# Optimization experiments

Measured on AMD Instinct MI355X. Metric: run time of the kernel, lower is better.

Reference implementation:

```python
import jax, jax.numpy as jnp
import numpy as np

T, B, INPUT_SIZE, NUM_NEURONS, OUTPUT_SIZE = 200, 256, 784, 1024, 10
TAU_M, V_REST, THRESH0, TAU_THRESH, BETA, DT = 20.0, -65.0, -50.0, 100.0, 5.0, 1.0


def setup_inputs() -> dict:
    key = jax.random.key(0)
    k1, k2, k3 = jax.random.split(key, 3)
    input_spikes = jax.random.uniform(k1, (T, B, INPUT_SIZE), dtype=jnp.float32)
    input_weights = jax.random.uniform(k2, (INPUT_SIZE, NUM_NEURONS), dtype=jnp.float32)
    # W_rec = -0.5 * (ones - eye): lateral inhibition buffer
    W_rec = -0.5 * (jnp.ones((NUM_NEURONS, NUM_NEURONS), jnp.float32) - jnp.eye(NUM_NEURONS, dtype=jnp.float32))
    output_weights = jax.random.uniform(k3, (NUM_NEURONS, OUTPUT_SIZE), dtype=jnp.float32)
    return {"input_spikes": input_spikes, "input_weights": input_weights,
            "W_rec": W_rec, "output_weights": output_weights}


def reference(input_spikes, input_weights, W_rec, output_weights):
    Bd = input_spikes.shape[1]
    n = input_weights.shape[1]
    mp0 = jnp.full((Bd, n), V_REST, jnp.float32)       # membrane potential
    th0 = jnp.full((Bd, n), THRESH0, jnp.float32)      # dynamic threshold
    h0 = jnp.zeros((Bd, n), jnp.float32)               # previous hidden spikes

    def step(carry, x_t):
        mp, th, prev = carry
        net = x_t @ input_weights + prev @ W_rec        # (B, n)
        mp = mp + (V_REST - mp) / TAU_M + net * DT
        spikes = (mp >= th).astype(jnp.float32)
        th = th + BETA * spikes - (th - THRESH0) / TAU_THRESH * DT
        mp = jnp.where(spikes > 0, V_REST, mp)          # reset on spike
        return (mp, th, spikes), spikes

    _, hidden_spikes = jax.lax.scan(step, (mp0, th0, h0), input_spikes)  # (T, B, n)
    spike_counts = hidden_spikes.sum(axis=0)            # (B, n)
    logits = spike_counts @ output_weights              # (B, out)
    return logits, hidden_spikes
```

## Files before the change

### kernel.cpp

```cpp
#include <hip/hip_runtime.h>


#define TT 200
#define BB 256
#define KK 784
#define NN 1024
#define OO 10

__device__ __forceinline__ float shfl_down64(float v, int d) {
  return __shfl_down(v, d, 64);
}

__global__ __launch_bounds__(256)
void gemm_net(const float* __restrict__ X, const float* __restrict__ W,
              float* __restrict__ C) {
  __shared__ float As[16][64];
  __shared__ float Bs[16][64];
  const int tid = threadIdx.x;
  const int m0 = blockIdx.x * 64;
  const int n0 = blockIdx.y * 64;
  const int tr = (tid >> 4) * 4;
  const int tc = (tid & 15) * 4;
  const int arow = tid >> 2;
  const int ak   = (tid & 3) * 4;
  const int brow = tid >> 4;
  const int bc   = (tid & 15) * 4;

  float acc[4][4] = {};

  for (int k0 = 0; k0 < KK; k0 += 16) {
    float4 av = *(const float4*)(X + (m0 + arow) * KK + k0 + ak);
    float4 bv = *(const float4*)(W + (k0 + brow) * NN + n0 + bc);
    __syncthreads();
    As[ak + 0][arow] = av.x;
    As[ak + 1][arow] = av.y;
    As[ak + 2][arow] = av.z;
    As[ak + 3][arow] = av.w;
    *(float4*)&Bs[brow][bc] = bv;
    __syncthreads();
#pragma unroll
    for (int k = 0; k < 16; ++k) {
      float4 a = *(const float4*)&As[k][tr];
      float4 b = *(const float4*)&Bs[k][tc];
      float aa[4] = {a.x, a.y, a.z, a.w};
      float bb[4] = {b.x, b.y, b.z, b.w};
#pragma unroll
      for (int i = 0; i < 4; ++i)
#pragma unroll
        for (int j = 0; j < 4; ++j)
          acc[i][j] = fmaf(aa[i], bb[j], acc[i][j]);
    }
  }
#pragma unroll
  for (int i = 0; i < 4; ++i) {
    float4 v = {acc[i][0], acc[i][1], acc[i][2], acc[i][3]};
    *(float4*)(C + (m0 + tr + i) * NN + n0 + tc) = v;
  }
}

__global__ __launch_bounds__(256)
void snn_scan(float* __restrict__ hid, const float* __restrict__ Wout,
              float* __restrict__ logits) {
  constexpr float V_REST = -65.0f, THRESH0 = -50.0f, TAU_M = 20.0f,
                  TAU_TH = 100.0f, BETA = 5.0f, DT = 1.0f;
  const int b = blockIdx.x;
  const int tid = threadIdx.x;
  __shared__ float s_part[4];
  __shared__ float s_log[4][OO];

  float mp[4], th[4], prev[4], cnt[4], net[4];
#pragma unroll
  for (int k = 0; k < 4; ++k) {
    mp[k] = V_REST; th[k] = THRESH0; prev[k] = 0.0f; cnt[k] = 0.0f;
  }
  float S = 0.0f;
  const int base = b * NN + tid;

#pragma unroll
  for (int k = 0; k < 4; ++k) net[k] = hid[base + k * 256];

  for (int t = 0; t < TT; ++t) {
    float local = 0.0f;
    float sp[4];
#pragma unroll
    for (int k = 0; k < 4; ++k) {
      float rec = -0.5f * (S - prev[k]);
      float nv  = net[k] + rec;
      float m   = mp[k] + (V_REST - mp[k]) / TAU_M;
      m = m + nv * DT;
      float s = (m >= th[k]) ? 1.0f : 0.0f;
      th[k] = (th[k] + BETA * s) - ((th[k] - THRESH0) / TAU_TH) * DT;
      mp[k] = (s > 0.0f) ? V_REST : m;
      cnt[k] += s;
      prev[k] = s;
      sp[k] = s;
      local += s;
    }
    const int off = t * (BB * NN) + base;
#pragma unroll
    for (int k = 0; k < 4; ++k) hid[off + k * 256] = sp[k];

    if (t + 1 < TT) {
      const int noff = (t + 1) * (BB * NN) + base;
#pragma unroll
      for (int k = 0; k < 4; ++k) net[k] = hid[noff + k * 256];
    }

#pragma unroll
    for (int d = 32; d > 0; d >>= 1) local += shfl_down64(local, d);
    __syncthreads();
    if ((tid & 63) == 0) s_part[tid >> 6] = local;
    __syncthreads();
    S = s_part[0] + s_part[1] + s_part[2] + s_part[3];
  }

  float lg[OO];
#pragma unroll
  for (int o = 0; o < OO; ++o) lg[o] = 0.0f;
#pragma unroll
  for (int k = 0; k < 4; ++k) {
    const int j = tid + k * 256;
#pragma unroll
    for (int o = 0; o < OO; ++o) lg[o] = fmaf(cnt[k], Wout[j * OO + o], lg[o]);
  }
#pragma unroll
  for (int o = 0; o < OO; ++o) {
    float v = lg[o];
#pragma unroll
    for (int d = 32; d > 0; d >>= 1) v += shfl_down64(v, d);
    if ((tid & 63) == 0) s_log[tid >> 6][o] = v;
  }
  __syncthreads();
  if (tid < OO)
    logits[b * OO + tid] =
        s_log[0][tid] + s_log[1][tid] + s_log[2][tid] + s_log[3][tid];
}

extern "C" void kernel_launch(void* const* d_in, const int* in_sizes, int n_in,
                              void* d_out, int out_size, void* d_ws,
                              size_t ws_size, hipStream_t stream) {
  const float* X    = (const float*)d_in[0];
  const float* Win  = (const float*)d_in[1];
  const float* Wout = (const float*)d_in[3];

  float* logits = (float*)d_out;
  float* hid    = (float*)d_out + BB * OO;

  dim3 g1(TT * BB / 64, NN / 64);
  gemm_net<<<g1, 256, 0, stream>>>(X, Win, hid);
  snn_scan<<<BB, 256, 0, stream>>>(hid, Wout, logits);
}
```

Baseline: 1.465 ms.

## Enlarge GEMM tiles to 128x128 and widen scan to one neuron per thread

The input-projection GEMM now computes 128x128 output tiles per block, with each thread holding an 8x8 register accumulator. This raises arithmetic intensity and cuts shared/global traffic per FMA, and the grid is reordered so N is the fast dimension. The scan kernel uses 1024 threads per batch row, one neuron each. It prefetches the net input two steps ahead, counts spikes with a wave ballot/popcount, and double-buffers the partial sums so each step needs only one barrier. The costs are higher register pressure in the GEMM and more waves per barrier in the scan.

```diff
diff --git a/kernel.cpp b/kernel.cpp
--- a/kernel.cpp
+++ b/kernel.cpp
@@ -7,133 +7,143 @@
 #define NN 1024
 #define OO 10
 
-__device__ __forceinline__ float shfl_down64(float v, int d) {
-  return __shfl_down(v, d, 64);
-}
-
 __global__ __launch_bounds__(256)
 void gemm_net(const float* __restrict__ X, const float* __restrict__ W,
               float* __restrict__ C) {
-  __shared__ float As[16][64];
-  __shared__ float Bs[16][64];
+  __shared__ float As[16][128];
+  __shared__ float Bs[16][128];
+  float4 (*As4)[32] = (float4(*)[32])As;
+  float4 (*Bs4)[32] = (float4(*)[32])Bs;
+
   const int tid = threadIdx.x;
-  const int m0 = blockIdx.x * 64;
-  const int n0 = blockIdx.y * 64;
-  const int tr = (tid >> 4) * 4;
-  const int tc = (tid & 15) * 4;
-  const int arow = tid >> 2;
-  const int ak   = (tid & 3) * 4;
-  const int brow = tid >> 4;
-  const int bc   = (tid & 15) * 4;
+  const int n0 = blockIdx.x * 128;
+  const int m0 = blockIdx.y * 128;
+  const int tx = tid & 15;
+  const int ty = tid >> 4;
+  const int arow = tid >> 1;
+  const int ak   = (tid & 1) * 8;
+  const int brow = tid >> 5;
+  const int bc   = (tid & 31) * 4;
 
-  float acc[4][4] = {};
+  float acc[2][2][4][4] = {};
 
   for (int k0 = 0; k0 < KK; k0 += 16) {
-    float4 av = *(const float4*)(X + (m0 + arow) * KK + k0 + ak);
-    float4 bv = *(const float4*)(W + (k0 + brow) * NN + n0 + bc);
+    const float* ap = X + (size_t)(m0 + arow) * KK + k0 + ak;
+    float4 a0 = *(const float4*)(ap);
+    float4 a1 = *(const float4*)(ap + 4);
+    float4 b0 = *(const float4*)(W + (size_t)(k0 + brow) * NN + n0 + bc);
+    float4 b1 = *(const float4*)(W + (size_t)(k0 + brow + 8) * NN + n0 + bc);
     __syncthreads();
-    As[ak + 0][arow] = av.x;
-    As[ak + 1][arow] = av.y;
-    As[ak + 2][arow] = av.z;
-    As[ak + 3][arow] = av.w;
-    *(float4*)&Bs[brow][bc] = bv;
+    As[ak + 0][arow] = a0.x;
+    As[ak + 1][arow] = a0.y;
+    As[ak + 2][arow] = a0.z;
+    As[ak + 3][arow] = a0.w;
+    As[ak + 4][arow] = a1.x;
+    As[ak + 5][arow] = a1.y;
+    As[ak + 6][arow] = a1.z;
+    As[ak + 7][arow] = a1.w;
+    *(float4*)&Bs[brow][bc] = b0;
+    *(float4*)&Bs[brow + 8][bc] = b1;
     __syncthreads();
 #pragma unroll
     for (int k = 0; k < 16; ++k) {
-      float4 a = *(const float4*)&As[k][tr];
-      float4 b = *(const float4*)&Bs[k][tc];
-      float aa[4] = {a.x, a.y, a.z, a.w};
-      float bb[4] = {b.x, b.y, b.z, b.w};
+      float4 A0 = As4[k][ty];
+      float4 A1 = As4[k][16 + ty];
+      float4 B0 = Bs4[k][tx];
+      float4 B1 = Bs4[k][16 + tx];
+      float a[2][4] = {{A0.x, A0.y, A0.z, A0.w}, {A1.x, A1.y, A1.z, A1.w}};
+      float b[2][4] = {{B0.x, B0.y, B0.z, B0.w}, {B1.x, B1.y, B1.z, B1.w}};
 #pragma unroll
-      for (int i = 0; i < 4; ++i)
+      for (int qi = 0; qi < 2; ++qi)
 #pragma unroll
-        for (int j = 0; j < 4; ++j)
-          acc[i][j] = fmaf(aa[i], bb[j], acc[i][j]);
+        for (int qj = 0; qj < 2; ++qj)
+#pragma unroll
+          for (int i = 0; i < 4; ++i)
+#pragma unroll
+            for (int j = 0; j < 4; ++j)
+              acc[qi][qj][i][j] = fmaf(a[qi][i], b[qj][j], acc[qi][qj][i][j]);
     }
   }
 #pragma unroll
-  for (int i = 0; i < 4; ++i) {
-    float4 v = {acc[i][0], acc[i][1], acc[i][2], acc[i][3]};
-    *(float4*)(C + (m0 + tr + i) * NN + n0 + tc) = v;
-  }
+  for (int qi = 0; qi < 2; ++qi)
+#pragma unroll
+    for (int i = 0; i < 4; ++i) {
+      const int r = m0 + qi * 64 + ty * 4 + i;
+#pragma unroll
+      for (int qj = 0; qj < 2; ++qj) {
+        float4 v = {acc[qi][qj][i][0], acc[qi][qj][i][1],
+                    acc[qi][qj][i][2], acc[qi][qj][i][3]};
+        *(float4*)(C + (size_t)r * NN + n0 + qj * 64 + tx * 4) = v;
+      }
+    }
 }
 
-__global__ __launch_bounds__(256)
+__global__ __launch_bounds__(1024)
 void snn_scan(float* __restrict__ hid, const float* __restrict__ Wout,
               float* __restrict__ logits) {
   constexpr float V_REST = -65.0f, THRESH0 = -50.0f, TAU_M = 20.0f,
                   TAU_TH = 100.0f, BETA = 5.0f, DT = 1.0f;
   const int b = blockIdx.x;
   const int tid = threadIdx.x;
-  __shared__ float s_part[4];
-  __shared__ float s_log[4][OO];
+  const int wave = tid >> 6, lane = tid & 63;
+  __shared__ float s_part[2][16];
+  __shared__ float s_log[16][OO];
 
-  float mp[4], th[4], prev[4], cnt[4], net[4];
-#pragma unroll
-  for (int k = 0; k < 4; ++k) {
-    mp[k] = V_REST; th[k] = THRESH0; prev[k] = 0.0f; cnt[k] = 0.0f;
-  }
+  float mp = V_REST, th = THRESH0, prev = 0.0f, cnt = 0.0f;
   float S = 0.0f;
-  const int base = b * NN + tid;
+  const size_t base = (size_t)b * NN + tid;
+  const size_t STEP = (size_t)BB * NN;
 
-#pragma unroll
-  for (int k = 0; k < 4; ++k) net[k] = hid[base + k * 256];
+  float netc = hid[base];
+  float netn = hid[STEP + base];
 
   for (int t = 0; t < TT; ++t) {
-    float local = 0.0f;
-    float sp[4];
-#pragma unroll
-    for (int k = 0; k < 4; ++k) {
-      float rec = -0.5f * (S - prev[k]);
-      float nv  = net[k] + rec;
-      float m   = mp[k] + (V_REST - mp[k]) / TAU_M;
-      m = m + nv * DT;
-      float s = (m >= th[k]) ? 1.0f : 0.0f;
-      th[k] = (th[k] + BETA * s) - ((th[k] - THRESH0) / TAU_TH) * DT;
-      mp[k] = (s > 0.0f) ? V_REST : m;
-      cnt[k] += s;
-      prev[k] = s;
-      sp[k] = s;
-      local += s;
-    }
-    const int off = t * (BB * NN) + base;
-#pragma unroll
-    for (int k = 0; k < 4; ++k) hid[off + k * 256] = sp[k];
+    float rec = -0.5f * (S - prev);
+    float nv = netc + rec;
+    float m = mp + (V_REST - mp) / TAU_M;
+    m = m + nv * DT;
+    bool spk = (m >= th);
+    float s = spk ? 1.0f : 0.0f;
+    th = (th + BETA * s) - ((th - THRESH0) / TAU_TH) * DT;
+    mp = spk ? V_REST : m;
+    cnt += s;
+    prev = s;
+    hid[(size_t)t * STEP + base] = s;
 
-    if (t + 1 < TT) {
-      const int noff = (t + 1) * (BB * NN) + base;
-#pragma unroll
-      for (int k = 0; k < 4; ++k) net[k] = hid[noff + k * 256];
-    }
+    float netf = 0.0f;
+    if (t + 2 < TT) netf = hid[(size_t)(t + 2) * STEP + base];
+    netc = netn;
+    netn = netf;
 
-#pragma unroll
-    for (int d = 32; d > 0; d >>= 1) local += shfl_down64(local, d);
+    unsigned long long bal = __ballot(spk);
+    if (lane == 0) s_part[t & 1][wave] = (float)__popcll(bal);
     __syncthreads();
-    if ((tid & 63) == 0) s_part[tid >> 6] = local;
-    __syncthreads();
-    S = s_part[0] + s_part[1] + s_part[2] + s_part[3];
+    const float* sp = s_part[t & 1];
+    float4 p0 = *(const float4*)(sp + 0);
+    float4 p1 = *(const float4*)(sp + 4);
+    float4 p2 = *(const float4*)(sp + 8);
+    float4 p3 = *(const float4*)(sp + 12);
+    S = ((p0.x + p0.y) + (p0.z + p0.w)) + ((p1.x + p1.y) + (p1.z + p1.w)) +
+        ((p2.x + p2.y) + (p2.z + p2.w)) + ((p3.x + p3.y) + (p3.z + p3.w));
   }
 
   float lg[OO];
 #pragma unroll
-  for (int o = 0; o < OO; ++o) lg[o] = 0.0f;
-#pragma unroll
-  for (int k = 0; k < 4; ++k) {
-    const int j = tid + k * 256;
-#pragma unroll
-    for (int o = 0; o < OO; ++o) lg[o] = fmaf(cnt[k], Wout[j * OO + o], lg[o]);
-  }
+  for (int o = 0; o < OO; ++o) lg[o] = cnt * Wout[(size_t)tid * OO + o];
 #pragma unroll
   for (int o = 0; o < OO; ++o) {
     float v = lg[o];
 #pragma unroll
-    for (int d = 32; d > 0; d >>= 1) v += shfl_down64(v, d);
-    if ((tid & 63) == 0) s_log[tid >> 6][o] = v;
+    for (int d = 32; d > 0; d >>= 1) v += __shfl_down(v, d, 64);
+    if (lane == 0) s_log[wave][o] = v;
   }
   __syncthreads();
-  if (tid < OO)
-    logits[b * OO + tid] =
-        s_log[0][tid] + s_log[1][tid] + s_log[2][tid] + s_log[3][tid];
+  if (tid < OO) {
+    float v = 0.0f;
+#pragma unroll
+    for (int w = 0; w < 16; ++w) v += s_log[w][tid];
+    logits[(size_t)b * OO + tid] = v;
+  }
 }
 
 extern "C" void kernel_launch(void* const* d_in, const int* in_sizes, int n_in,
@@ -146,7 +156,7 @@
   float* logits = (float*)d_out;
   float* hid    = (float*)d_out + BB * OO;
 
-  dim3 g1(TT * BB / 64, NN / 64);
+  dim3 g1(NN / 128, TT * BB / 128);
   gemm_net<<<g1, 256, 0, stream>>>(X, Win, hid);
-  snn_scan<<<BB, 256, 0, stream>>>(hid, Wout, logits);
+  snn_scan<<<BB, 1024, 0, stream>>>(hid, Wout, logits);
 }
```

After: 1.244 ms. -15.0%, faster.
